# Kernel tuning notes

Hardware: AMD Instinct MI355X
Metric: run time of the kernel (lower is better)

The kernel has to match this reference:

```python
import jax, jax.numpy as jnp
import numpy as np

T = 262144          # total packed neighbor tokens
D_IN, D_H, D_OUT = 128, 256, 128
N_SETS = 8192


def setup_inputs() -> dict:
    key = jax.random.key(0)
    k1, k2, k3, k4, k5, k6 = jax.random.split(key, 6)
    x = jax.random.normal(k1, (T, D_IN), dtype=jnp.float32)
    segment_ids = jnp.sort(jax.random.randint(k2, (T,), 0, N_SETS))
    # phi params (torch Linear: y = x @ W.T + b); store as [in, out] for einsum
    s1 = 1.0 / np.sqrt(D_IN)
    s2 = 1.0 / np.sqrt(D_H)
    W1 = jax.random.uniform(k3, (D_IN, D_H), jnp.float32, -s1, s1)
    b1 = jax.random.uniform(k4, (D_H,), jnp.float32, -s1, s1)
    W2 = jax.random.uniform(k5, (D_H, D_OUT), jnp.float32, -s2, s2)
    b2 = jax.random.uniform(k6, (D_OUT,), jnp.float32, -s2, s2)
    return {"x": x, "segment_ids": segment_ids, "num_segments": N_SETS,
            "W1": W1, "b1": b1, "W2": W2, "b2": b2}


def reference(x, segment_ids, num_segments, W1, b1, W2, b2):
    # phi: Linear -> ReLU -> Linear -> ReLU, applied to every packed token
    h = jax.nn.relu(x @ W1 + b1)            # [T, D_H]
    h = jax.nn.relu(h @ W2 + b2)            # [T, D_OUT]
    # per-set mean pool (segment mean over ragged sets)
    sums = jax.ops.segment_sum(h, segment_ids, num_segments=num_segments)  # [N, D_OUT]
    counts = jax.ops.segment_sum(jnp.ones((h.shape[0],), h.dtype), segment_ids,
                                 num_segments=num_segments)                 # [N]
    out = sums / jnp.maximum(counts, 1.0)[:, None]
    return out
```

## Files before the change

kernel.cpp:

```cpp
#include <hip/hip_runtime.h>

#define D_IN 128
#define D_H 256
#define D_OUT 128
#define N_SETS 8192
#define T_TOTAL 262144

typedef short short8 __attribute__((ext_vector_type(8)));
typedef short short4v __attribute__((ext_vector_type(4)));
typedef float floatx4 __attribute__((ext_vector_type(4)));

typedef const __attribute__((address_space(1))) unsigned int gu32;
typedef __attribute__((address_space(3))) unsigned int lu32;

__device__ inline unsigned short f32_bf16(float f) {
    unsigned int u = __float_as_uint(f);
    u += 0x7FFFu + ((u >> 16) & 1u);
    return (unsigned short)(u >> 16);
}

__global__ void setup_kernel(const float* __restrict__ W1, const float* __restrict__ W2,
                             unsigned short* __restrict__ W1s, unsigned short* __restrict__ W2s,
                             float4* __restrict__ out4, float4* __restrict__ cnt4) {
    if (blockIdx.x < 32) {
        int t = blockIdx.x * 256 + threadIdx.x;
        int l = t & 63;
        int f = (t >> 6) & 63;
        int q = l >> 4, r = l & 15;
        if (t < 4096) {
            int nt = f >> 2, c = f & 3;
            int k0 = c * 32 + q * 8, n = nt * 16 + r;
            unsigned short v[8];
#pragma unroll
            for (int j = 0; j < 8; j++) v[j] = f32_bf16(W1[(k0 + j) * D_H + n]);
#pragma unroll
            for (int j = 0; j < 8; j++) W1s[f * 512 + l * 8 + j] = v[j];
        } else {
            int nt = f >> 3, c = f & 7;
            int k0 = c * 32 + q * 8, n = nt * 16 + r;
            unsigned short v[8];
#pragma unroll
            for (int j = 0; j < 8; j++) v[j] = f32_bf16(W2[(k0 + j) * D_OUT + n]);
#pragma unroll
            for (int j = 0; j < 8; j++) W2s[f * 512 + l * 8 + j] = v[j];
        }
    } else {
        int i = (blockIdx.x - 32) * 256 + threadIdx.x;
        float4 z = make_float4(0.f, 0.f, 0.f, 0.f);
        if (i < 262144) out4[i] = z;
        else if (i < 264192) cnt4[i - 262144] = z;
    }
}

__global__ __launch_bounds__(768, 3) void ds_main(
    const float* __restrict__ x, const int* __restrict__ seg,
    const unsigned short* __restrict__ W1s, const float* __restrict__ b1,
    const unsigned short* __restrict__ W2s, const float* __restrict__ b2,
    float* __restrict__ out, float* __restrict__ counts)
{
    __shared__ __align__(16) unsigned short wbuf[128 * 512];
    __shared__ __align__(16) unsigned short slabs[12][1280];
    __shared__ int ssegs[12][32];

    const int tid = threadIdx.x;
    const int wave = tid >> 6, lane = tid & 63;
    const int r = lane & 15, q = lane >> 4;
    const int tok0 = blockIdx.x * 384 + wave * 32;
    const bool active = (tok0 < T_TOTAL);

    if (wave < 8) {
#pragma unroll
        for (int i = 0; i < 8; i++) {
            __builtin_amdgcn_global_load_lds((gu32*)(W1s + i * 4096 + tid * 8),
                                             (lu32*)(wbuf + i * 4096 + tid * 8), 16, 0, 0);
            __builtin_amdgcn_global_load_lds((gu32*)(W2s + i * 4096 + tid * 8),
                                             (lu32*)(wbuf + 32768 + i * 4096 + tid * 8), 16, 0, 0);
        }
    }

    unsigned short* slab = slabs[wave];
    int* sseg = ssegs[wave];

    short8 xfb[2][4];
    if (active) {
        if (lane < 32) sseg[lane] = seg[tok0 + lane];
#pragma unroll
        for (int mt = 0; mt < 2; mt++) {
            const float* xp = x + (size_t)(tok0 + mt * 16 + r) * D_IN + q * 8;
#pragma unroll
            for (int c = 0; c < 4; c++) {
                float4 v0 = *(const float4*)(xp + c * 32);
                float4 v1 = *(const float4*)(xp + c * 32 + 4);
                short8 w;
                w[0] = (short)f32_bf16(v0.x); w[1] = (short)f32_bf16(v0.y);
                w[2] = (short)f32_bf16(v0.z); w[3] = (short)f32_bf16(v0.w);
                w[4] = (short)f32_bf16(v1.x); w[5] = (short)f32_bf16(v1.y);
                w[6] = (short)f32_bf16(v1.z); w[7] = (short)f32_bf16(v1.w);
                xfb[mt][c] = w;
            }
        }
    }

    floatx4 acc2[8][2];
#pragma unroll
    for (int i = 0; i < 8; i++) {
        acc2[i][0] = (floatx4){0.f, 0.f, 0.f, 0.f};
        acc2[i][1] = (floatx4){0.f, 0.f, 0.f, 0.f};
    }

    __syncthreads();
    if (!active) return;

#pragma unroll
    for (int kc = 0; kc < 8; kc++) {
#pragma unroll
        for (int t = 0; t < 2; t++) {
            const int nt = kc * 2 + t;
            short8 w1f[4];
#pragma unroll
            for (int c = 0; c < 4; c++)
                w1f[c] = *(const short8*)(wbuf + (nt * 4 + c) * 512 + lane * 8);
            floatx4 b1v = *(const floatx4*)(b1 + nt * 16 + q * 4);
            floatx4 acc1[2];
            acc1[0] = (floatx4){0.f, 0.f, 0.f, 0.f};
            acc1[1] = (floatx4){0.f, 0.f, 0.f, 0.f};
#pragma unroll
            for (int c = 0; c < 4; c++) {
                acc1[0] = __builtin_amdgcn_mfma_f32_16x16x32_bf16(w1f[c], xfb[0][c], acc1[0], 0, 0, 0);
                acc1[1] = __builtin_amdgcn_mfma_f32_16x16x32_bf16(w1f[c], xfb[1][c], acc1[1], 0, 0, 0);
            }
#pragma unroll
            for (int mt = 0; mt < 2; mt++) {
                short4v pk;
#pragma unroll
                for (int i = 0; i < 4; i++)
                    pk[i] = (short)f32_bf16(fmaxf(acc1[mt][i] + b1v[i], 0.f));
                *(short4v*)(slab + (mt * 16 + r) * 40 + t * 16 + q * 4) = pk;
            }
        }
        short8 a2[2];
        a2[0] = *(const short8*)(slab + r * 40 + q * 8);
        a2[1] = *(const short8*)(slab + (16 + r) * 40 + q * 8);
#pragma unroll
        for (int nt2 = 0; nt2 < 8; nt2++) {
            short8 bw = *(const short8*)(wbuf + (64 + nt2 * 8 + kc) * 512 + lane * 8);
            acc2[nt2][0] = __builtin_amdgcn_mfma_f32_16x16x32_bf16(a2[0], bw, acc2[nt2][0], 0, 0, 0);
            acc2[nt2][1] = __builtin_amdgcn_mfma_f32_16x16x32_bf16(a2[1], bw, acc2[nt2][1], 0, 0, 0);
        }
    }

    if (lane < 32) {
        int s = sseg[lane];
        if (lane == 0 || sseg[lane - 1] != s) {
            int len = 1;
            for (int u = lane + 1; u < 32 && sseg[u] == s; ++u) ++len;
            atomicAdd(&counts[s], (float)len);
        }
    }

    int sid[8];
#pragma unroll
    for (int e = 0; e < 8; e++) sid[e] = sseg[q * 8 + e];

    float* h2 = (float*)slab;
#pragma unroll
    for (int nt2 = 0; nt2 < 8; nt2++) {
        const float bias = b2[nt2 * 16 + r];
#pragma unroll
        for (int mt = 0; mt < 2; mt++) {
            floatx4 v;
#pragma unroll
            for (int i = 0; i < 4; i++) v[i] = fmaxf(acc2[nt2][mt][i] + bias, 0.f);
            *(floatx4*)(h2 + r * 36 + mt * 16 + q * 4) = v;
        }
        floatx4 v0 = *(const floatx4*)(h2 + r * 36 + q * 8);
        floatx4 v1 = *(const floatx4*)(h2 + r * 36 + q * 8 + 4);
        const int col = nt2 * 16 + r;
        float sum = v0[0];
#pragma unroll
        for (int e = 1; e < 8; e++) {
            float v = (e < 4) ? v0[e] : v1[e - 4];
            if (sid[e] != sid[e - 1]) {
                atomicAdd(&out[(size_t)sid[e - 1] * D_OUT + col], sum);
                sum = 0.f;
            }
            sum += v;
        }
        atomicAdd(&out[(size_t)sid[7] * D_OUT + col], sum);
    }
}

__global__ void div_kernel(float4* __restrict__ out4, const float* __restrict__ counts) {
    int i = blockIdx.x * 256 + threadIdx.x;
    float inv = 1.f / fmaxf(counts[i >> 5], 1.f);
    float4 v = out4[i];
    v.x *= inv; v.y *= inv; v.z *= inv; v.w *= inv;
    out4[i] = v;
}

extern "C" void kernel_launch(void* const* d_in, const int* in_sizes, int n_in,
                              void* d_out, int out_size, void* d_ws, size_t ws_size,
                              hipStream_t stream) {
    const float* x  = (const float*)d_in[0];
    const int* seg  = (const int*)d_in[1];
    const float* W1 = (const float*)d_in[3];
    const float* b1 = (const float*)d_in[4];
    const float* W2 = (const float*)d_in[5];
    const float* b2 = (const float*)d_in[6];
    float* out = (float*)d_out;

    float* counts       = (float*)d_ws;
    unsigned short* W1s = (unsigned short*)((char*)d_ws + 32768);
    unsigned short* W2s = (unsigned short*)((char*)d_ws + 32768 + 65536);

    hipLaunchKernelGGL(setup_kernel, dim3(1064), dim3(256), 0, stream,
                       W1, W2, W1s, W2s, (float4*)out, (float4*)counts);
    hipLaunchKernelGGL(ds_main, dim3(683), dim3(768), 0, stream,
                       x, seg, W1s, b1, W2s, b2, out, counts);
    hipLaunchKernelGGL(div_kernel, dim3(1024), dim3(256), 0, stream,
                       (float4*)out, counts);
}
```

Measured before the change: 270.3 us.

## Switch MLP to 32x32x16 MFMA with permlane swaps instead of LDS staging

Rewrites both GEMMs to use 32x32x16 bf16 MFMA tiles, repacking the weight layouts to match. The layer-1 output is moved into the layer-2 operand layout with v_permlane32_swap in registers, and the LDS slab round-trips for hidden activations and the pooling epilogue are removed. It also uses hardware packed bf16 conversion and replaces the zeroing grid with hipMemsetAsync. The aim is to cut LDS traffic and conversion instructions and to issue fewer, larger MFMAs. In exchange it raises register pressure (floatx16 accumulators) and depends on the permlane lane mapping being correct.

```diff
diff --git a/kernel.cpp b/kernel.cpp
--- a/kernel.cpp
+++ b/kernel.cpp
@@ -7,11 +7,14 @@
 #define T_TOTAL 262144
 
 typedef short short8 __attribute__((ext_vector_type(8)));
-typedef short short4v __attribute__((ext_vector_type(4)));
 typedef float floatx4 __attribute__((ext_vector_type(4)));
+typedef float floatx16 __attribute__((ext_vector_type(16)));
+typedef unsigned int uint4v __attribute__((ext_vector_type(4)));
 
 typedef const __attribute__((address_space(1))) unsigned int gu32;
 typedef __attribute__((address_space(3))) unsigned int lu32;
+
+union U8 { uint4v u; short8 s; };
 
 __device__ inline unsigned short f32_bf16(float f) {
     unsigned int u = __float_as_uint(f);
@@ -20,35 +23,28 @@
 }
 
 __global__ void setup_kernel(const float* __restrict__ W1, const float* __restrict__ W2,
-                             unsigned short* __restrict__ W1s, unsigned short* __restrict__ W2s,
-                             float4* __restrict__ out4, float4* __restrict__ cnt4) {
-    if (blockIdx.x < 32) {
-        int t = blockIdx.x * 256 + threadIdx.x;
-        int l = t & 63;
-        int f = (t >> 6) & 63;
-        int q = l >> 4, r = l & 15;
-        if (t < 4096) {
-            int nt = f >> 2, c = f & 3;
-            int k0 = c * 32 + q * 8, n = nt * 16 + r;
-            unsigned short v[8];
-#pragma unroll
-            for (int j = 0; j < 8; j++) v[j] = f32_bf16(W1[(k0 + j) * D_H + n]);
-#pragma unroll
-            for (int j = 0; j < 8; j++) W1s[f * 512 + l * 8 + j] = v[j];
-        } else {
-            int nt = f >> 3, c = f & 7;
-            int k0 = c * 32 + q * 8, n = nt * 16 + r;
-            unsigned short v[8];
-#pragma unroll
-            for (int j = 0; j < 8; j++) v[j] = f32_bf16(W2[(k0 + j) * D_OUT + n]);
-#pragma unroll
-            for (int j = 0; j < 8; j++) W2s[f * 512 + l * 8 + j] = v[j];
-        }
+                             unsigned short* __restrict__ W1s, unsigned short* __restrict__ W2s) {
+    int t = blockIdx.x * 256 + threadIdx.x;
+    int l = t & 63;
+    int f = t >> 6;
+    int hl = l >> 5, c31 = l & 31;
+    if (f < 64) {
+        int nt = f >> 3, c = f & 7;
+        int k0 = c * 16 + hl * 8, n = nt * 32 + c31;
+        unsigned short v[8];
+#pragma unroll
+        for (int j = 0; j < 8; j++) v[j] = f32_bf16(W1[(k0 + j) * D_H + n]);
+#pragma unroll
+        for (int j = 0; j < 8; j++) W1s[f * 512 + l * 8 + j] = v[j];
     } else {
-        int i = (blockIdx.x - 32) * 256 + threadIdx.x;
-        float4 z = make_float4(0.f, 0.f, 0.f, 0.f);
-        if (i < 262144) out4[i] = z;
-        else if (i < 264192) cnt4[i - 262144] = z;
+        int g = f - 64;
+        int o = g >> 4, c2 = g & 15;
+        int k0 = c2 * 16 + hl * 8, n = o * 32 + c31;
+        unsigned short v[8];
+#pragma unroll
+        for (int j = 0; j < 8; j++) v[j] = f32_bf16(W2[(k0 + j) * D_OUT + n]);
+#pragma unroll
+        for (int j = 0; j < 8; j++) W2s[g * 512 + l * 8 + j] = v[j];
     }
 }
 
@@ -59,12 +55,11 @@
     float* __restrict__ out, float* __restrict__ counts)
 {
     __shared__ __align__(16) unsigned short wbuf[128 * 512];
-    __shared__ __align__(16) unsigned short slabs[12][1280];
     __shared__ int ssegs[12][32];
 
     const int tid = threadIdx.x;
     const int wave = tid >> 6, lane = tid & 63;
-    const int r = lane & 15, q = lane >> 4;
+    const int hl = lane >> 5, c31 = lane & 31;
     const int tok0 = blockIdx.x * 384 + wave * 32;
     const bool active = (tok0 < T_TOTAL);
 
@@ -78,74 +73,70 @@
         }
     }
 
-    unsigned short* slab = slabs[wave];
     int* sseg = ssegs[wave];
 
-    short8 xfb[2][4];
+    short8 xfa[8];
     if (active) {
         if (lane < 32) sseg[lane] = seg[tok0 + lane];
-#pragma unroll
-        for (int mt = 0; mt < 2; mt++) {
-            const float* xp = x + (size_t)(tok0 + mt * 16 + r) * D_IN + q * 8;
-#pragma unroll
-            for (int c = 0; c < 4; c++) {
-                float4 v0 = *(const float4*)(xp + c * 32);
-                float4 v1 = *(const float4*)(xp + c * 32 + 4);
-                short8 w;
-                w[0] = (short)f32_bf16(v0.x); w[1] = (short)f32_bf16(v0.y);
-                w[2] = (short)f32_bf16(v0.z); w[3] = (short)f32_bf16(v0.w);
-                w[4] = (short)f32_bf16(v1.x); w[5] = (short)f32_bf16(v1.y);
-                w[6] = (short)f32_bf16(v1.z); w[7] = (short)f32_bf16(v1.w);
-                xfb[mt][c] = w;
-            }
-        }
-    }
-
-    floatx4 acc2[8][2];
-#pragma unroll
-    for (int i = 0; i < 8; i++) {
-        acc2[i][0] = (floatx4){0.f, 0.f, 0.f, 0.f};
-        acc2[i][1] = (floatx4){0.f, 0.f, 0.f, 0.f};
-    }
+        const float* xp = x + (size_t)(tok0 + c31) * D_IN + hl * 8;
+#pragma unroll
+        for (int c = 0; c < 8; c++) {
+            float4 v0 = *(const float4*)(xp + c * 16);
+            float4 v1 = *(const float4*)(xp + c * 16 + 4);
+            unsigned int p0, p1, p2, p3;
+            asm("v_cvt_pk_bf16_f32 %0, %1, %2" : "=v"(p0) : "v"(v0.x), "v"(v0.y));
+            asm("v_cvt_pk_bf16_f32 %0, %1, %2" : "=v"(p1) : "v"(v0.z), "v"(v0.w));
+            asm("v_cvt_pk_bf16_f32 %0, %1, %2" : "=v"(p2) : "v"(v1.x), "v"(v1.y));
+            asm("v_cvt_pk_bf16_f32 %0, %1, %2" : "=v"(p3) : "v"(v1.z), "v"(v1.w));
+            U8 u; u.u = (uint4v){p0, p1, p2, p3};
+            xfa[c] = u.s;
+        }
+    }
+
+    floatx16 acc2[4];
+#pragma unroll
+    for (int o = 0; o < 4; o++)
+#pragma unroll
+        for (int i = 0; i < 16; i++) acc2[o][i] = 0.f;
 
     __syncthreads();
     if (!active) return;
 
 #pragma unroll
-    for (int kc = 0; kc < 8; kc++) {
-#pragma unroll
-        for (int t = 0; t < 2; t++) {
-            const int nt = kc * 2 + t;
-            short8 w1f[4];
-#pragma unroll
-            for (int c = 0; c < 4; c++)
-                w1f[c] = *(const short8*)(wbuf + (nt * 4 + c) * 512 + lane * 8);
-            floatx4 b1v = *(const floatx4*)(b1 + nt * 16 + q * 4);
-            floatx4 acc1[2];
-            acc1[0] = (floatx4){0.f, 0.f, 0.f, 0.f};
-            acc1[1] = (floatx4){0.f, 0.f, 0.f, 0.f};
-#pragma unroll
-            for (int c = 0; c < 4; c++) {
-                acc1[0] = __builtin_amdgcn_mfma_f32_16x16x32_bf16(w1f[c], xfb[0][c], acc1[0], 0, 0, 0);
-                acc1[1] = __builtin_amdgcn_mfma_f32_16x16x32_bf16(w1f[c], xfb[1][c], acc1[1], 0, 0, 0);
+    for (int nt = 0; nt < 8; nt++) {
+        floatx16 acc1;
+#pragma unroll
+        for (int i = 0; i < 16; i++) acc1[i] = 0.f;
+#pragma unroll
+        for (int c = 0; c < 8; c++) {
+            short8 wf = *(const short8*)(wbuf + (nt * 8 + c) * 512 + lane * 8);
+            acc1 = __builtin_amdgcn_mfma_f32_32x32x16_bf16(wf, xfa[c], acc1, 0, 0, 0);
+        }
+        float v[16];
+#pragma unroll
+        for (int g = 0; g < 4; g++) {
+            floatx4 bv = *(const floatx4*)(b1 + nt * 32 + g * 8 + hl * 4);
+#pragma unroll
+            for (int i = 0; i < 4; i++) v[g * 4 + i] = fmaxf(acc1[g * 4 + i] + bv[i], 0.f);
+        }
+        unsigned int pk[8];
+#pragma unroll
+        for (int p = 0; p < 8; p++)
+            asm("v_cvt_pk_bf16_f32 %0, %1, %2" : "=v"(pk[p]) : "v"(v[2 * p]), "v"(v[2 * p + 1]));
+#pragma unroll
+        for (int s = 0; s < 2; s++) {
+            unsigned int d0 = pk[s * 4 + 0], d2 = pk[s * 4 + 2];
+            asm("v_permlane32_swap_b32 %0, %1" : "+v"(d0), "+v"(d2));
+            unsigned int d1 = pk[s * 4 + 1], d3 = pk[s * 4 + 3];
+            asm("v_permlane32_swap_b32 %0, %1" : "+v"(d1), "+v"(d3));
+            U8 u; u.u = (uint4v){d0, d1, d2, d3};
+            const short8 hf = u.s;
+            const int c2 = nt * 2 + s;
+#pragma unroll
+            for (int o = 0; o < 4; o++) {
+                short8 bw = *(const short8*)(wbuf + (64 + o * 16 + c2) * 512 + lane * 8);
+                acc2[o] = __builtin_amdgcn_mfma_f32_32x32x16_bf16(hf, bw, acc2[o], 0, 0, 0);
             }
-#pragma unroll
-            for (int mt = 0; mt < 2; mt++) {
-                short4v pk;
-#pragma unroll
-                for (int i = 0; i < 4; i++)
-                    pk[i] = (short)f32_bf16(fmaxf(acc1[mt][i] + b1v[i], 0.f));
-                *(short4v*)(slab + (mt * 16 + r) * 40 + t * 16 + q * 4) = pk;
-            }
-        }
-        short8 a2[2];
-        a2[0] = *(const short8*)(slab + r * 40 + q * 8);
-        a2[1] = *(const short8*)(slab + (16 + r) * 40 + q * 8);
-#pragma unroll
-        for (int nt2 = 0; nt2 < 8; nt2++) {
-            short8 bw = *(const short8*)(wbuf + (64 + nt2 * 8 + kc) * 512 + lane * 8);
-            acc2[nt2][0] = __builtin_amdgcn_mfma_f32_16x16x32_bf16(a2[0], bw, acc2[nt2][0], 0, 0, 0);
-            acc2[nt2][1] = __builtin_amdgcn_mfma_f32_16x16x32_bf16(a2[1], bw, acc2[nt2][1], 0, 0, 0);
         }
     }
 
@@ -158,35 +149,37 @@
         }
     }
 
-    int sid[8];
-#pragma unroll
-    for (int e = 0; e < 8; e++) sid[e] = sseg[q * 8 + e];
-
-    float* h2 = (float*)slab;
-#pragma unroll
-    for (int nt2 = 0; nt2 < 8; nt2++) {
-        const float bias = b2[nt2 * 16 + r];
-#pragma unroll
-        for (int mt = 0; mt < 2; mt++) {
-            floatx4 v;
-#pragma unroll
-            for (int i = 0; i < 4; i++) v[i] = fmaxf(acc2[nt2][mt][i] + bias, 0.f);
-            *(floatx4*)(h2 + r * 36 + mt * 16 + q * 4) = v;
-        }
-        floatx4 v0 = *(const floatx4*)(h2 + r * 36 + q * 8);
-        floatx4 v1 = *(const floatx4*)(h2 + r * 36 + q * 8 + 4);
-        const int col = nt2 * 16 + r;
-        float sum = v0[0];
-#pragma unroll
-        for (int e = 1; e < 8; e++) {
-            float v = (e < 4) ? v0[e] : v1[e - 4];
+    int sid[16];
+#pragma unroll
+    for (int e = 0; e < 16; e++) sid[e] = sseg[hl * 16 + e];
+
+#pragma unroll
+    for (int o = 0; o < 4; o++) {
+        const float bias = b2[o * 32 + c31];
+        float val[16];
+#pragma unroll
+        for (int r = 0; r < 16; r++) val[r] = fmaxf(acc2[o][r] + bias, 0.f);
+        float st[16];
+#pragma unroll
+        for (int i = 0; i < 4; i++) {
+            float a = val[i], b = val[8 + i];
+            asm("v_permlane32_swap_b32 %0, %1" : "+v"(a), "+v"(b));
+            st[i] = a; st[4 + i] = b;
+            float c = val[4 + i], d = val[12 + i];
+            asm("v_permlane32_swap_b32 %0, %1" : "+v"(c), "+v"(d));
+            st[8 + i] = c; st[12 + i] = d;
+        }
+        const int col = o * 32 + c31;
+        float sum = st[0];
+#pragma unroll
+        for (int e = 1; e < 16; e++) {
             if (sid[e] != sid[e - 1]) {
                 atomicAdd(&out[(size_t)sid[e - 1] * D_OUT + col], sum);
                 sum = 0.f;
             }
-            sum += v;
-        }
-        atomicAdd(&out[(size_t)sid[7] * D_OUT + col], sum);
+            sum += st[e];
+        }
+        atomicAdd(&out[(size_t)sid[15] * D_OUT + col], sum);
     }
 }
 
@@ -213,8 +206,10 @@
     unsigned short* W1s = (unsigned short*)((char*)d_ws + 32768);
     unsigned short* W2s = (unsigned short*)((char*)d_ws + 32768 + 65536);
 
-    hipLaunchKernelGGL(setup_kernel, dim3(1064), dim3(256), 0, stream,
-                       W1, W2, W1s, W2s, (float4*)out, (float4*)counts);
+    hipMemsetAsync(out, 0, (size_t)N_SETS * D_OUT * sizeof(float), stream);
+    hipMemsetAsync(counts, 0, (size_t)N_SETS * sizeof(float), stream);
+    hipLaunchKernelGGL(setup_kernel, dim3(32), dim3(256), 0, stream,
+                       W1, W2, W1s, W2s);
     hipLaunchKernelGGL(ds_main, dim3(683), dim3(768), 0, stream,
                        x, seg, W1s, b1, W2s, b2, out, counts);
     hipLaunchKernelGGL(div_kernel, dim3(1024), dim3(256), 0, stream,
```

Measured after the change: 252.4 us. 1.07x faster.
